# Kernel tuning notes

Measured on AMD Instinct MI355X. Metric: run time of the kernel, lower is better.

## Reference

```python
import math
import jax, jax.numpy as jnp
import numpy as np

B, S, H, NH = 8, 1024, 1024, 16
HD = H // NH  # head dim = 64

def setup_inputs() -> dict:
    key = jax.random.key(0)
    ks = jax.random.split(key, 4)
    scale = 1.0 / math.sqrt(H)
    return {
        "hidden_state": jax.random.normal(ks[0], (B, S, H), jnp.float32),
        "attention_mask": jnp.ones((B, 1, S), jnp.float32),
        "Wq": jax.random.normal(ks[1], (H, H), jnp.float32) * scale,
        "bq": jnp.zeros((H,), jnp.float32),
        "Wk": jax.random.normal(ks[2], (H, H), jnp.float32) * scale,
        "bk": jnp.zeros((H,), jnp.float32),
        "Wv": jax.random.normal(ks[3], (H, H), jnp.float32) * scale,
        "bv": jnp.zeros((H,), jnp.float32),
    }

def _split_heads(x):
    # [B,S,H] -> [B,NH,S,HD]
    return x.reshape(B, S, NH, HD).transpose(0, 2, 1, 3)

def reference(hidden_state, attention_mask, Wq, bq, Wk, bk, Wv, bv):
    q = _split_heads(hidden_state @ Wq.T + bq)
    k = _split_heads(hidden_state @ Wk.T + bk)
    v = _split_heads(hidden_state @ Wv.T + bv)
    scores = jnp.einsum("bhqd,bhkd->bhqk", q, k) / math.sqrt(HD)
    # mask [B,1,S] -> additive bias [B,1,S,1], broadcast over heads and keys
    bias = (1.0 - attention_mask)[..., None] * -10000.0
    scores = scores + bias
    probs = jax.nn.softmax(scores, axis=-1)  # dropout prob = 0.0 (eval)
    ctx = jnp.einsum("bhqk,bhkd->bhqd", probs, v)
    return ctx.transpose(0, 2, 1, 3).reshape(B, S, H)
```

## Files before the change

### kernel.cpp

```cpp
#include <hip/hip_runtime.h>
#include <hip/hip_bf16.h>


typedef __attribute__((ext_vector_type(8))) short bf16x8;
typedef __attribute__((ext_vector_type(4))) float f32x4;
typedef unsigned short u16;

#define NB 8
#define NS 1024
#define NH_ 16
#define HD_ 64
#define QKV_T (NB * NH_ * NS * HD_)
#define XN (8192 * 1024)
#define WN (1024 * 1024)
#define QSCL 0.180336880f

static __device__ __forceinline__ u16 f2bf(float f) {
    unsigned int u = __float_as_uint(f);
    u += 0x7FFFu + ((u >> 16) & 1u);
    return (u16)(u >> 16);
}

static __device__ __forceinline__ bf16x8 cvt8(const float* p) {
    float4 a = *(const float4*)p;
    float4 b = *(const float4*)(p + 4);
    union { bf16x8 v; u16 s[8]; } r;
    r.s[0] = f2bf(a.x); r.s[1] = f2bf(a.y); r.s[2] = f2bf(a.z); r.s[3] = f2bf(a.w);
    r.s[4] = f2bf(b.x); r.s[5] = f2bf(b.y); r.s[6] = f2bf(b.z); r.s[7] = f2bf(b.w);
    return r.v;
}

static __device__ __forceinline__ void async16(const u16* g, u16* l) {
    __builtin_amdgcn_global_load_lds((const __attribute__((address_space(1))) void*)g,
                                     (__attribute__((address_space(3))) void*)l,
                                     16, 0, 0);
}

static __device__ __forceinline__ unsigned int cvtpk(float a, float b) {
    unsigned int r;
    asm("v_cvt_pk_bf16_f32 %0, %1, %2" : "=v"(r) : "v"(a), "v"(b));
    return r;
}

__global__ __launch_bounds__(256) void cvt_pass(
    const float* __restrict__ X,
    const float* __restrict__ Wq, const float* __restrict__ Wk,
    const float* __restrict__ Wv,
    u16* __restrict__ Xb, u16* __restrict__ Wb)
{
    size_t i8 = ((size_t)blockIdx.x * 256 + threadIdx.x) * 8;
    if (i8 < XN) {
        *(bf16x8*)(Xb + i8) = cvt8(X + i8);
    } else {
        size_t j = i8 - XN;
        int w = (int)(j >> 20);
        const float* src = (w == 0) ? Wq : (w == 1) ? Wk : Wv;
        *(bf16x8*)(Wb + j) = cvt8(src + (j & (WN - 1)));
    }
}

#define GEMM2_LDS_BYTES 131072

__global__ __launch_bounds__(512, 2) void qkv_gemm_8ph(
    const u16* __restrict__ Xb, const u16* __restrict__ Wb,
    const float* __restrict__ bq, const float* __restrict__ bk,
    const float* __restrict__ bv,
    u16* __restrict__ qkv)
{
    extern __shared__ u16 sm[];

    const int tid  = threadIdx.x;
    const int lane = tid & 63;
    const int wid  = tid >> 6;
    const int l15  = lane & 15;
    const int quad = lane >> 4;
    const int sw   = l15 & 7;
    const int wr   = wid >> 2;
    const int wc   = wid & 3;

    const int bid = blockIdx.x;
    const int xcd = bid & 7;
    const int loc = bid >> 3;
    const int m0  = ((xcd & 3) * 8 + loc / 6) * 256;
    const int n0  = ((xcd >> 2) * 6 + loc % 6) * 256;

    const u16* Ap = Xb + (size_t)m0 * 1024;
    const u16* Bp = Wb + (size_t)n0 * 1024;

    int offG[2], offL[2];
#pragma unroll
    for (int it = 0; it < 2; ++it) {
        int idx = it * 512 + tid;
        int lr = idx >> 3, kc = idx & 7;
        offG[it] = lr * 1024 + ((kc ^ (lr & 7)) * 8);
        offL[it] = idx * 8;
    }

    const int arow = wr * 64 + l15;
    const int brow = wc * 32 + l15;

    f32x4 acc[2][2][4][2];
#pragma unroll
    for (int qm = 0; qm < 2; ++qm)
#pragma unroll
        for (int qn = 0; qn < 2; ++qn)
#pragma unroll
            for (int mi = 0; mi < 4; ++mi)
#pragma unroll
                for (int ni = 0; ni < 2; ++ni)
                    acc[qm][qn][mi][ni] = (f32x4){0.f, 0.f, 0.f, 0.f};

    bf16x8 a[4][2], b[2][2];

#define STG_A(BUF, H, T) do { if ((T) < 16) { \
    _Pragma("unroll") for (int it = 0; it < 2; ++it) \
        async16(Ap + (size_t)(H) * 131072 + (T) * 64 + offG[it], \
                sm + ((BUF) * 4 + (H)) * 8192 + offL[it]); } } while (0)
#define STG_B(BUF, H, T) do { if ((T) < 16) { \
    _Pragma("unroll") for (int it = 0; it < 2; ++it) \
        async16(Bp + (size_t)(H) * 131072 + (T) * 64 + offG[it], \
                sm + ((BUF) * 4 + 2 + (H)) * 8192 + offL[it]); } } while (0)
#define LDA(BUF, QM) do { \
    _Pragma("unroll") for (int mi = 0; mi < 4; ++mi) { \
        _Pragma("unroll") for (int kk = 0; kk < 2; ++kk) \
            a[mi][kk] = *(const bf16x8*)&sm[((BUF) * 4 + (QM)) * 8192 + \
                (arow + mi * 16) * 64 + (((kk * 4 + quad) ^ sw) * 8)]; } } while (0)
#define LDB(BUF, QN) do { \
    _Pragma("unroll") for (int ni = 0; ni < 2; ++ni) { \
        _Pragma("unroll") for (int kk = 0; kk < 2; ++kk) \
            b[ni][kk] = *(const bf16x8*)&sm[((BUF) * 4 + 2 + (QN)) * 8192 + \
                (brow + ni * 16) * 64 + (((kk * 4 + quad) ^ sw) * 8)]; } } while (0)
#define MM(QM, QN) do { __builtin_amdgcn_s_setprio(1); \
    _Pragma("unroll") for (int kk = 0; kk < 2; ++kk) \
    _Pragma("unroll") for (int mi = 0; mi < 4; ++mi) \
    _Pragma("unroll") for (int ni = 0; ni < 2; ++ni) \
        acc[QM][QN][mi][ni] = __builtin_amdgcn_mfma_f32_16x16x32_bf16( \
            a[mi][kk], b[ni][kk], acc[QM][QN][mi][ni], 0, 0, 0); \
    __builtin_amdgcn_s_setprio(0); } while (0)
#define BAR asm volatile("s_barrier" ::: "memory")
#define WAITV4 asm volatile("s_waitcnt vmcnt(4)" ::: "memory")
#define WAITV0 asm volatile("s_waitcnt vmcnt(0)" ::: "memory")

    STG_A(0, 0, 0); STG_B(0, 1, 0); STG_A(0, 1, 0);
    STG_B(0, 0, 0); STG_A(1, 0, 1); STG_B(1, 1, 1);
    WAITV4;
    BAR;

    for (int jj = 0; jj < 8; ++jj) {
        const int j0 = jj * 2, j1 = j0 + 1;
        LDA(0, 0); LDB(0, 0); STG_A(1, 1, j0 + 1); MM(0, 0); BAR;
        LDB(0, 1);            STG_B(1, 0, j0 + 1); MM(0, 1); BAR;
        LDA(0, 1);            STG_A(0, 0, j0 + 2); MM(1, 1); BAR;
        LDB(0, 0);            STG_B(0, 1, j0 + 2); MM(1, 0);
        if (jj == 7) { WAITV0; } else { WAITV4; }
        BAR;
        LDA(1, 0); LDB(1, 0); STG_A(0, 1, j1 + 1); MM(0, 0); BAR;
        LDB(1, 1);            STG_B(0, 0, j1 + 1); MM(0, 1); BAR;
        LDA(1, 1);            STG_A(1, 0, j1 + 2); MM(1, 1); BAR;
        LDB(1, 0);            STG_B(1, 1, j1 + 2); MM(1, 0);
        if (jj < 7) { WAITV4; BAR; }
    }

    const int which = n0 >> 10;
    const int ncol0 = n0 & 1023;
    const int batch = m0 >> 10;
    const int mrow0 = m0 & 1023;
    const float* bias = (which == 0) ? bq : (which == 1) ? bk : bv;
    const float scl   = (which == 0) ? QSCL : 1.0f;

    if (which == 2) {
#pragma unroll
        for (int qm = 0; qm < 2; ++qm)
#pragma unroll
            for (int qn = 0; qn < 2; ++qn)
#pragma unroll
                for (int ni = 0; ni < 2; ++ni) {
                    int col = ncol0 + qn * 128 + wc * 32 + ni * 16 + l15;
                    float bia = bias[col];
                    int h = col >> 6;
                    int d = col & 63;
                    size_t base = (size_t)((2 * NB + batch) * NH_ + h) * (NS * HD_);
#pragma unroll
                    for (int mi = 0; mi < 4; ++mi) {
                        int s = mrow0 + qm * 128 + wr * 64 + mi * 16 + quad * 4;
                        ushort4 pk;
                        pk.x = f2bf(acc[qm][qn][mi][ni][0] + bia);
                        pk.y = f2bf(acc[qm][qn][mi][ni][1] + bia);
                        pk.z = f2bf(acc[qm][qn][mi][ni][2] + bia);
                        pk.w = f2bf(acc[qm][qn][mi][ni][3] + bia);
                        *(ushort4*)&qkv[base + (size_t)d * NS + s] = pk;
                    }
                }
    } else {
        u16* Cs = sm;
        const size_t tb = (size_t)((which * NB + batch) * NH_) * (NS * HD_);
        const int h0 = ncol0 >> 6;
        __syncthreads();
#pragma unroll
        for (int qm = 0; qm < 2; ++qm) {
            if (qm) __syncthreads();
#pragma unroll
            for (int qn = 0; qn < 2; ++qn)
#pragma unroll
                for (int ni = 0; ni < 2; ++ni) {
                    int col = qn * 128 + wc * 32 + ni * 16 + l15;
                    float bia = bias[ncol0 + col];
#pragma unroll
                    for (int mi = 0; mi < 4; ++mi)
#pragma unroll
                        for (int r = 0; r < 4; ++r)
                            Cs[(wr * 64 + mi * 16 + quad * 4 + r) * 264 + col] =
                                f2bf((acc[qm][qn][mi][ni][r] + bia) * scl);
                }
            __syncthreads();
#pragma unroll
            for (int it = 0; it < 8; ++it) {
                int idx = it * 512 + tid;
                int lr = idx >> 5;
                int c  = idx & 31;
                int s  = mrow0 + qm * 128 + lr;
                int h  = h0 + (c >> 3);
                *(uint4*)&qkv[tb + (size_t)h * (NS * HD_) + (size_t)s * HD_ + (c & 7) * 8] =
                    *(const uint4*)&Cs[lr * 264 + c * 8];
            }
        }
    }
#undef STG_A
#undef STG_B
#undef LDA
#undef LDB
#undef MM
#undef BAR
#undef WAITV4
#undef WAITV0
}

__global__ __launch_bounds__(256) void qkv_gemm_f32(
    const float* __restrict__ X,
    const float* __restrict__ Wq, const float* __restrict__ bq,
    const float* __restrict__ Wk, const float* __restrict__ bk,
    const float* __restrict__ Wv, const float* __restrict__ bv,
    u16* __restrict__ qkv)
{
    __shared__ u16 As[128 * 72];
    __shared__ u16 Bs[128 * 72];
    const int tid  = threadIdx.x;
    const int lane = tid & 63;
    const int wid  = tid >> 6;
    const int l15  = lane & 15;
    const int quad = lane >> 4;
    const int wm   = (wid >> 1) * 64;
    const int wn   = (wid & 1) * 64;
    const int m0   = blockIdx.x * 128;
    const int nb   = blockIdx.y * 128;
    const int which = nb >> 10;
    const int ncol0 = nb & 1023;
    const float* W    = (which == 0) ? Wq : (which == 1) ? Wk : Wv;
    const float* bias = (which == 0) ? bq : (which == 1) ? bk : bv;
    const float scl   = (which == 0) ? QSCL : 1.0f;

    f32x4 acc[4][4];
#pragma unroll
    for (int mi = 0; mi < 4; ++mi)
#pragma unroll
        for (int ni = 0; ni < 4; ++ni) acc[mi][ni] = (f32x4){0.f, 0.f, 0.f, 0.f};

    for (int kt = 0; kt < 16; ++kt) {
#pragma unroll
        for (int it = 0; it < 4; ++it) {
            int idx = it * 256 + tid;
            int row = idx >> 3, c = idx & 7;
            *(bf16x8*)&As[row * 72 + c * 8] = cvt8(&X[(size_t)(m0 + row) * 1024 + kt * 64 + c * 8]);
            *(bf16x8*)&Bs[row * 72 + c * 8] = cvt8(&W[(size_t)(ncol0 + row) * 1024 + kt * 64 + c * 8]);
        }
        __syncthreads();
#pragma unroll
        for (int kk = 0; kk < 2; ++kk) {
            bf16x8 a[4], b[4];
#pragma unroll
            for (int mi = 0; mi < 4; ++mi)
                a[mi] = *(const bf16x8*)&As[(wm + mi * 16 + l15) * 72 + kk * 32 + quad * 8];
#pragma unroll
            for (int ni = 0; ni < 4; ++ni)
                b[ni] = *(const bf16x8*)&Bs[(wn + ni * 16 + l15) * 72 + kk * 32 + quad * 8];
#pragma unroll
            for (int mi = 0; mi < 4; ++mi)
#pragma unroll
                for (int ni = 0; ni < 4; ++ni)
                    acc[mi][ni] = __builtin_amdgcn_mfma_f32_16x16x32_bf16(
                        a[mi], b[ni], acc[mi][ni], 0, 0, 0);
        }
        __syncthreads();
    }
#pragma unroll
    for (int ni = 0; ni < 4; ++ni) {
        int nn = ncol0 + wn + ni * 16 + l15;
        float bia = bias[nn];
        int h = nn >> 6;
        int d = nn & 63;
#pragma unroll
        for (int mi = 0; mi < 4; ++mi) {
#pragma unroll
            for (int r = 0; r < 4; ++r) {
                int rg    = m0 + wm + mi * 16 + quad * 4 + r;
                int batch = rg >> 10;
                int s     = rg & 1023;
                size_t base = (size_t)((which * NB + batch) * NH_ + h) * (NS * HD_);
                size_t off  = (which == 2) ? base + (size_t)d * NS + s
                                           : base + (size_t)s * HD_ + d;
                qkv[off] = f2bf((acc[mi][ni][r] + bia) * scl);
            }
        }
    }
}

#define ATTN_LDS_BYTES 69632

__global__ __launch_bounds__(512, 4) void attn(
    const u16* __restrict__ qkv, float* __restrict__ out)
{
    extern __shared__ u16 asm_[];
    u16* KsB  = asm_;
    u16* VTsB = asm_ + 8192;
    u16* Ps   = asm_ + 16384;

    const int tid  = threadIdx.x;
    const int lane = tid & 63;
    const int wid  = tid >> 6;
    const int l15  = lane & 15;
    const int quad = lane >> 4;
    const int sw   = l15 & 7;

    const int id    = blockIdx.x;
    const int hb    = (id & 7) * 16 + (id >> 5);
    const int q0    = ((id >> 3) & 3) * 256;
    const int h     = hb & 15;
    const int batch = hb >> 4;

    const size_t headoff = (size_t)(batch * NH_ + h) * (NS * HD_);
    const u16* Qg = qkv + headoff;
    const u16* Kg = qkv + (size_t)QKV_T + headoff;
    const u16* Vt = qkv + (size_t)2 * QKV_T + headoff;

    {
    }
    const int srow = tid >> 3, skc = tid & 7;
    const int skcs = (skc ^ (srow & 7)) * 8;
    const u16* kp = Kg + (size_t)srow * 64 + skcs;
    const u16* vp = Vt + (size_t)srow * NS + skcs;

    bf16x8 aq[2][2];
#pragma unroll
    for (int f = 0; f < 2; ++f)
#pragma unroll
        for (int kk = 0; kk < 2; ++kk)
            aq[f][kk] = *(const bf16x8*)&Qg[(size_t)(q0 + wid * 32 + f * 16 + l15) * 64 + kk * 32 + quad * 8];

    async16(kp, KsB + tid * 8);
    async16(vp, VTsB + tid * 8);
    __syncthreads();

    float lsum[2] = {0.f, 0.f};
    f32x4 o[2][4];
#pragma unroll
    for (int f = 0; f < 2; ++f)
#pragma unroll
        for (int ni = 0; ni < 4; ++ni) o[f][ni] = (f32x4){0.f, 0.f, 0.f, 0.f};

    for (int kt = 0; kt < 16; ++kt) {
        const u16* Kc = KsB + (kt & 1) * 4096;
        const u16* Vc = VTsB + (kt & 1) * 4096;

        if (kt < 15) {
            u16* Kn = KsB + ((kt & 1) ^ 1) * 4096;
            u16* Vn = VTsB + ((kt & 1) ^ 1) * 4096;
            async16(kp + (size_t)(kt + 1) * 4096, Kn + tid * 8);
            async16(vp + (size_t)(kt + 1) * 64, Vn + tid * 8);
        }

        f32x4 sfr[2][4];
        __builtin_amdgcn_s_setprio(1);
#pragma unroll
        for (int ni = 0; ni < 4; ++ni) {
            bf16x8 b0 = *(const bf16x8*)&Kc[(ni * 16 + l15) * 64 + ((quad ^ sw) * 8)];
            bf16x8 b1 = *(const bf16x8*)&Kc[(ni * 16 + l15) * 64 + (((4 + quad) ^ sw) * 8)];
#pragma unroll
            for (int f = 0; f < 2; ++f) {
                f32x4 sa = (f32x4){0.f, 0.f, 0.f, 0.f};
                sa = __builtin_amdgcn_mfma_f32_16x16x32_bf16(b0, aq[f][0], sa, 0, 0, 0);
                sa = __builtin_amdgcn_mfma_f32_16x16x32_bf16(b1, aq[f][1], sa, 0, 0, 0);
                sfr[f][ni] = sa;
            }
        }
        __builtin_amdgcn_s_setprio(0);

#pragma unroll
        for (int f = 0; f < 2; ++f)
#pragma unroll
            for (int ni = 0; ni < 4; ++ni) {
                float p0 = __builtin_amdgcn_exp2f(sfr[f][ni][0]);
                float p1 = __builtin_amdgcn_exp2f(sfr[f][ni][1]);
                float p2 = __builtin_amdgcn_exp2f(sfr[f][ni][2]);
                float p3 = __builtin_amdgcn_exp2f(sfr[f][ni][3]);
                lsum[f] += (p0 + p1) + (p2 + p3);
                uint2 pk;
                pk.x = cvtpk(p0, p1);
                pk.y = cvtpk(p2, p3);
                *(uint2*)&Ps[(wid * 32 + f * 16 + l15) * 72 + ni * 16 + quad * 4] = pk;
            }

        __builtin_amdgcn_s_setprio(1);
#pragma unroll
        for (int kk = 0; kk < 2; ++kk) {
            bf16x8 ap[2];
#pragma unroll
            for (int f = 0; f < 2; ++f)
                ap[f] = *(const bf16x8*)&Ps[(wid * 32 + f * 16 + l15) * 72 + kk * 32 + quad * 8];
#pragma unroll
            for (int ni = 0; ni < 4; ++ni) {
                bf16x8 bv_ = *(const bf16x8*)&Vc[(ni * 16 + l15) * 64 + (((kk * 4 + quad) ^ sw) * 8)];
#pragma unroll
                for (int f = 0; f < 2; ++f)
                    o[f][ni] = __builtin_amdgcn_mfma_f32_16x16x32_bf16(ap[f], bv_, o[f][ni], 0, 0, 0);
            }
        }
        __builtin_amdgcn_s_setprio(0);
        __syncthreads();
    }

#pragma unroll
    for (int f = 0; f < 2; ++f) {
        lsum[f] += __shfl_xor(lsum[f], 16, 64);
        lsum[f] += __shfl_xor(lsum[f], 32, 64);
    }

#pragma unroll
    for (int f = 0; f < 2; ++f) {
        float inv[4];
#pragma unroll
        for (int r = 0; r < 4; ++r)
            inv[r] = 1.0f / __shfl(lsum[f], quad * 4 + r, 64);
#pragma unroll
        for (int ni = 0; ni < 4; ++ni)
#pragma unroll
            for (int r = 0; r < 4; ++r) {
                int row = wid * 32 + f * 16 + quad * 4 + r;
                out[(size_t)(batch * NS + q0 + row) * 1024 + h * 64 + ni * 16 + l15] =
                    o[f][ni][r] * inv[r];
            }
    }
}

extern "C" void kernel_launch(void* const* d_in, const int* in_sizes, int n_in,
                              void* d_out, int out_size, void* d_ws, size_t ws_size,
                              hipStream_t stream) {
    const float* X  = (const float*)d_in[0];
    const float* Wq = (const float*)d_in[2];
    const float* bq = (const float*)d_in[3];
    const float* Wk = (const float*)d_in[4];
    const float* bk = (const float*)d_in[5];
    const float* Wv = (const float*)d_in[6];
    const float* bv = (const float*)d_in[7];
    float* outp = (float*)d_out;

    u16* qkv = (u16*)d_ws;
    u16* Xb  = (u16*)((char*)d_ws + (size_t)QKV_T * 3 * 2);
    u16* Wb  = Xb + XN;
    const size_t need = (size_t)QKV_T * 3 * 2 + (size_t)XN * 2 + (size_t)3 * WN * 2;

    static bool attr_done = false;
    if (!attr_done) {
        (void)hipFuncSetAttribute((const void*)qkv_gemm_8ph,
                                  hipFuncAttributeMaxDynamicSharedMemorySize,
                                  GEMM2_LDS_BYTES);
        (void)hipFuncSetAttribute((const void*)attn,
                                  hipFuncAttributeMaxDynamicSharedMemorySize,
                                  ATTN_LDS_BYTES);
        attr_done = true;
    }

    if (ws_size >= need) {
        cvt_pass<<<(XN + 3 * WN) / 8 / 256, 256, 0, stream>>>(X, Wq, Wk, Wv, Xb, Wb);
        qkv_gemm_8ph<<<384, 512, GEMM2_LDS_BYTES, stream>>>(Xb, Wb, bq, bk, bv, qkv);
    } else {
        qkv_gemm_f32<<<dim3(64, 24), 256, 0, stream>>>(X, Wq, bq, Wk, bk, Wv, bv, qkv);
    }
    attn<<<512, 512, ATTN_LDS_BYTES, stream>>>(qkv, outp);
}
```

Measured before the change: 200.9 us.

## Halve QKV GEMM tile width to 256x128 and double grid to fix wave quantization

Changes the QKV projection GEMM block tile from 256x256 to 256x128, doubling the grid to 768 blocks and shrinking LDS to 96KB. B staging, fragment loads, MFMA accumulators, wait counts and both epilogues are adjusted to the narrower tile. The intent is to remove the partial last wave of the 384-block launch and balance work across CUs. The cost is lower data reuse per block, since A tiles are reloaded twice as often.

```diff
diff --git a/kernel.cpp b/kernel.cpp
--- a/kernel.cpp
+++ b/kernel.cpp
@@ -59,7 +59,7 @@
     }
 }
 
-#define GEMM2_LDS_BYTES 131072
+#define GEMM2_LDS_BYTES 98304
 
 __global__ __launch_bounds__(512, 2) void qkv_gemm_8ph(
     const u16* __restrict__ Xb, const u16* __restrict__ Wb,
@@ -81,69 +81,67 @@
     const int bid = blockIdx.x;
     const int xcd = bid & 7;
     const int loc = bid >> 3;
-    const int m0  = ((xcd & 3) * 8 + loc / 6) * 256;
-    const int n0  = ((xcd >> 2) * 6 + loc % 6) * 256;
+    const int m0  = ((xcd & 3) * 8 + loc / 12) * 256;
+    const int n0  = (((xcd >> 2) * 12 + loc % 12)) * 128;
 
     const u16* Ap = Xb + (size_t)m0 * 1024;
     const u16* Bp = Wb + (size_t)n0 * 1024;
 
-    int offG[2], offL[2];
+    int offGA[2], offLA[2];
 #pragma unroll
     for (int it = 0; it < 2; ++it) {
         int idx = it * 512 + tid;
         int lr = idx >> 3, kc = idx & 7;
-        offG[it] = lr * 1024 + ((kc ^ (lr & 7)) * 8);
-        offL[it] = idx * 8;
-    }
+        offGA[it] = lr * 1024 + ((kc ^ (lr & 7)) * 8);
+        offLA[it] = idx * 8;
+    }
+    const int blr = tid >> 3, bkc = tid & 7;
+    const int offGB = blr * 1024 + ((bkc ^ (blr & 7)) * 8);
+    const int offLB = tid * 8;
 
     const int arow = wr * 64 + l15;
-    const int brow = wc * 32 + l15;
-
-    f32x4 acc[2][2][4][2];
+    const int brow = wc * 16 + l15;
+
+    f32x4 acc[2][2][4];
 #pragma unroll
     for (int qm = 0; qm < 2; ++qm)
 #pragma unroll
         for (int qn = 0; qn < 2; ++qn)
 #pragma unroll
             for (int mi = 0; mi < 4; ++mi)
-#pragma unroll
-                for (int ni = 0; ni < 2; ++ni)
-                    acc[qm][qn][mi][ni] = (f32x4){0.f, 0.f, 0.f, 0.f};
-
-    bf16x8 a[4][2], b[2][2];
+                acc[qm][qn][mi] = (f32x4){0.f, 0.f, 0.f, 0.f};
+
+    bf16x8 a[4][2], b[2];
 
 #define STG_A(BUF, H, T) do { if ((T) < 16) { \
     _Pragma("unroll") for (int it = 0; it < 2; ++it) \
-        async16(Ap + (size_t)(H) * 131072 + (T) * 64 + offG[it], \
-                sm + ((BUF) * 4 + (H)) * 8192 + offL[it]); } } while (0)
+        async16(Ap + (size_t)(H) * 131072 + (T) * 64 + offGA[it], \
+                sm + (BUF) * 24576 + (H) * 8192 + offLA[it]); } } while (0)
 #define STG_B(BUF, H, T) do { if ((T) < 16) { \
-    _Pragma("unroll") for (int it = 0; it < 2; ++it) \
-        async16(Bp + (size_t)(H) * 131072 + (T) * 64 + offG[it], \
-                sm + ((BUF) * 4 + 2 + (H)) * 8192 + offL[it]); } } while (0)
+    async16(Bp + (size_t)(H) * 65536 + (T) * 64 + offGB, \
+            sm + (BUF) * 24576 + 16384 + (H) * 4096 + offLB); } } while (0)
 #define LDA(BUF, QM) do { \
     _Pragma("unroll") for (int mi = 0; mi < 4; ++mi) { \
         _Pragma("unroll") for (int kk = 0; kk < 2; ++kk) \
-            a[mi][kk] = *(const bf16x8*)&sm[((BUF) * 4 + (QM)) * 8192 + \
+            a[mi][kk] = *(const bf16x8*)&sm[(BUF) * 24576 + (QM) * 8192 + \
                 (arow + mi * 16) * 64 + (((kk * 4 + quad) ^ sw) * 8)]; } } while (0)
 #define LDB(BUF, QN) do { \
-    _Pragma("unroll") for (int ni = 0; ni < 2; ++ni) { \
-        _Pragma("unroll") for (int kk = 0; kk < 2; ++kk) \
-            b[ni][kk] = *(const bf16x8*)&sm[((BUF) * 4 + 2 + (QN)) * 8192 + \
-                (brow + ni * 16) * 64 + (((kk * 4 + quad) ^ sw) * 8)]; } } while (0)
+    _Pragma("unroll") for (int kk = 0; kk < 2; ++kk) \
+        b[kk] = *(const bf16x8*)&sm[(BUF) * 24576 + 16384 + (QN) * 4096 + \
+            brow * 64 + (((kk * 4 + quad) ^ sw) * 8)]; } while (0)
 #define MM(QM, QN) do { __builtin_amdgcn_s_setprio(1); \
     _Pragma("unroll") for (int kk = 0; kk < 2; ++kk) \
     _Pragma("unroll") for (int mi = 0; mi < 4; ++mi) \
-    _Pragma("unroll") for (int ni = 0; ni < 2; ++ni) \
-        acc[QM][QN][mi][ni] = __builtin_amdgcn_mfma_f32_16x16x32_bf16( \
-            a[mi][kk], b[ni][kk], acc[QM][QN][mi][ni], 0, 0, 0); \
+        acc[QM][QN][mi] = __builtin_amdgcn_mfma_f32_16x16x32_bf16( \
+            a[mi][kk], b[kk], acc[QM][QN][mi], 0, 0, 0); \
     __builtin_amdgcn_s_setprio(0); } while (0)
 #define BAR asm volatile("s_barrier" ::: "memory")
-#define WAITV4 asm volatile("s_waitcnt vmcnt(4)" ::: "memory")
+#define WAITV3 asm volatile("s_waitcnt vmcnt(3)" ::: "memory")
 #define WAITV0 asm volatile("s_waitcnt vmcnt(0)" ::: "memory")
 
     STG_A(0, 0, 0); STG_B(0, 1, 0); STG_A(0, 1, 0);
     STG_B(0, 0, 0); STG_A(1, 0, 1); STG_B(1, 1, 1);
-    WAITV4;
+    WAITV3;
     BAR;
 
     for (int jj = 0; jj < 8; ++jj) {
@@ -152,13 +150,13 @@
         LDB(0, 1);            STG_B(1, 0, j0 + 1); MM(0, 1); BAR;
         LDA(0, 1);            STG_A(0, 0, j0 + 2); MM(1, 1); BAR;
         LDB(0, 0);            STG_B(0, 1, j0 + 2); MM(1, 0);
-        if (jj == 7) { WAITV0; } else { WAITV4; }
+        if (jj == 7) { WAITV0; } else { WAITV3; }
         BAR;
         LDA(1, 0); LDB(1, 0); STG_A(0, 1, j1 + 1); MM(0, 0); BAR;
         LDB(1, 1);            STG_B(0, 0, j1 + 1); MM(0, 1); BAR;
         LDA(1, 1);            STG_A(1, 0, j1 + 2); MM(1, 1); BAR;
         LDB(1, 0);            STG_B(1, 1, j1 + 2); MM(1, 0);
-        if (jj < 7) { WAITV4; BAR; }
+        if (jj < 7) { WAITV3; BAR; }
     }
 
     const int which = n0 >> 10;
@@ -172,25 +170,23 @@
 #pragma unroll
         for (int qm = 0; qm < 2; ++qm)
 #pragma unroll
-            for (int qn = 0; qn < 2; ++qn)
-#pragma unroll
-                for (int ni = 0; ni < 2; ++ni) {
-                    int col = ncol0 + qn * 128 + wc * 32 + ni * 16 + l15;
-                    float bia = bias[col];
-                    int h = col >> 6;
-                    int d = col & 63;
-                    size_t base = (size_t)((2 * NB + batch) * NH_ + h) * (NS * HD_);
-#pragma unroll
-                    for (int mi = 0; mi < 4; ++mi) {
-                        int s = mrow0 + qm * 128 + wr * 64 + mi * 16 + quad * 4;
-                        ushort4 pk;
-                        pk.x = f2bf(acc[qm][qn][mi][ni][0] + bia);
-                        pk.y = f2bf(acc[qm][qn][mi][ni][1] + bia);
-                        pk.z = f2bf(acc[qm][qn][mi][ni][2] + bia);
-                        pk.w = f2bf(acc[qm][qn][mi][ni][3] + bia);
-                        *(ushort4*)&qkv[base + (size_t)d * NS + s] = pk;
-                    }
+            for (int qn = 0; qn < 2; ++qn) {
+                int col = ncol0 + qn * 64 + wc * 16 + l15;
+                float bia = bias[col];
+                int h = col >> 6;
+                int d = col & 63;
+                size_t base = (size_t)((2 * NB + batch) * NH_ + h) * (NS * HD_);
+#pragma unroll
+                for (int mi = 0; mi < 4; ++mi) {
+                    int s = mrow0 + qm * 128 + wr * 64 + mi * 16 + quad * 4;
+                    ushort4 pk;
+                    pk.x = f2bf(acc[qm][qn][mi][0] + bia);
+                    pk.y = f2bf(acc[qm][qn][mi][1] + bia);
+                    pk.z = f2bf(acc[qm][qn][mi][2] + bia);
+                    pk.w = f2bf(acc[qm][qn][mi][3] + bia);
+                    *(ushort4*)&qkv[base + (size_t)d * NS + s] = pk;
                 }
+            }
     } else {
         u16* Cs = sm;
         const size_t tb = (size_t)((which * NB + batch) * NH_) * (NS * HD_);
@@ -200,28 +196,26 @@
         for (int qm = 0; qm < 2; ++qm) {
             if (qm) __syncthreads();
 #pragma unroll
-            for (int qn = 0; qn < 2; ++qn)
-#pragma unroll
-                for (int ni = 0; ni < 2; ++ni) {
-                    int col = qn * 128 + wc * 32 + ni * 16 + l15;
-                    float bia = bias[ncol0 + col];
-#pragma unroll
-                    for (int mi = 0; mi < 4; ++mi)
-#pragma unroll
-                        for (int r = 0; r < 4; ++r)
-                            Cs[(wr * 64 + mi * 16 + quad * 4 + r) * 264 + col] =
-                                f2bf((acc[qm][qn][mi][ni][r] + bia) * scl);
-                }
+            for (int qn = 0; qn < 2; ++qn) {
+                int col = qn * 64 + wc * 16 + l15;
+                float bia = bias[ncol0 + col];
+#pragma unroll
+                for (int mi = 0; mi < 4; ++mi)
+#pragma unroll
+                    for (int r = 0; r < 4; ++r)
+                        Cs[(wr * 64 + mi * 16 + quad * 4 + r) * 132 + col] =
+                            f2bf((acc[qm][qn][mi][r] + bia) * scl);
+            }
             __syncthreads();
 #pragma unroll
-            for (int it = 0; it < 8; ++it) {
+            for (int it = 0; it < 4; ++it) {
                 int idx = it * 512 + tid;
-                int lr = idx >> 5;
-                int c  = idx & 31;
+                int lr = idx >> 4;
+                int c  = idx & 15;
                 int s  = mrow0 + qm * 128 + lr;
                 int h  = h0 + (c >> 3);
                 *(uint4*)&qkv[tb + (size_t)h * (NS * HD_) + (size_t)s * HD_ + (c & 7) * 8] =
-                    *(const uint4*)&Cs[lr * 264 + c * 8];
+                    *(const uint4*)&Cs[lr * 132 + c * 8];
             }
         }
     }
@@ -231,7 +225,7 @@
 #undef LDB
 #undef MM
 #undef BAR
-#undef WAITV4
+#undef WAITV3
 #undef WAITV0
 }
 
@@ -342,8 +336,6 @@
     const u16* Kg = qkv + (size_t)QKV_T + headoff;
     const u16* Vt = qkv + (size_t)2 * QKV_T + headoff;
 
-    {
-    }
     const int srow = tid >> 3, skc = tid & 7;
     const int skcs = (skc ^ (srow & 7)) * 8;
     const u16* kp = Kg + (size_t)srow * 64 + skcs;
@@ -481,7 +473,7 @@
 
     if (ws_size >= need) {
         cvt_pass<<<(XN + 3 * WN) / 8 / 256, 256, 0, stream>>>(X, Wq, Wk, Wv, Xb, Wb);
-        qkv_gemm_8ph<<<384, 512, GEMM2_LDS_BYTES, stream>>>(Xb, Wb, bq, bk, bv, qkv);
+        qkv_gemm_8ph<<<768, 512, GEMM2_LDS_BYTES, stream>>>(Xb, Wb, bq, bk, bv, qkv);
     } else {
         qkv_gemm_f32<<<dim3(64, 24), 256, 0, stream>>>(X, Wq, bq, Wk, bk, Wv, bv, qkv);
     }
```

Result: slower. 205.5 us (+2.3%).
